# Kernel optimization log

Hardware: AMD Instinct MI355X
Metric: run time of the kernel (lower is better)

The kernel has to match this reference:

```python
import jax, jax.numpy as jnp
import numpy as np

BETA_MIN = 0.1
BETA_MAX = 20.0


def _Beta(t):
    # integral of linear beta schedule
    return BETA_MIN * t + 0.5 * (BETA_MAX - BETA_MIN) * t ** 2


def setup_inputs() -> dict:
    key = jax.random.key(0)
    k1, k2, k3, k4, k5 = jax.random.split(key, 5)
    B, K, D = 4096, 128, 256
    x = jax.random.normal(k1, (B, D), dtype=jnp.float32)
    t = jax.random.uniform(k2, (B,), dtype=jnp.float32)
    centers = jax.random.normal(k3, (K, D), dtype=jnp.float32)
    # keep stds positive and well-conditioned
    stds = 0.5 + 0.5 * jax.random.uniform(k4, (K, D), dtype=jnp.float32)
    # positive mixture weights (original only requires positivity, takes log)
    weights = 0.1 + jax.random.uniform(k5, (K,), dtype=jnp.float32)
    return {"x": x, "t": t, "centers": centers, "stds": stds, "weights": weights}


def reference(x, t, centers, stds, weights):
    ndim = centers.shape[1]

    def log_prob(xx):
        Bt = _Beta(t)[:, None, None]                 # [B,1,1]
        a = jnp.exp(-Bt / 2)
        centers_t = a * centers[None]                # [B,K,D]
        var_t = jnp.exp(-Bt) * stds[None] ** 2 + 1.0 - jnp.exp(-Bt)  # [B,K,D]
        diff = xx[:, None, :] - centers_t            # [B,K,D]
        # NOTE: faithful to source, which uses ndim/2 * sum(log(2*pi*var)) (not 1/2)
        lp = (-(diff ** 2) / (2.0 * var_t)).sum(-1) \
             - (ndim / 2) * jnp.log(2.0 * jnp.pi * var_t).sum(-1)    # [B,K]
        lp = lp + jnp.log(weights)[None, :]
        return jax.scipy.special.logsumexp(lp, axis=1)               # [B]

    grad_log_prob = jax.grad(lambda xx: log_prob(xx).sum())(x)       # [B,D]
    Bt = _Beta(t)[:, None]                                           # [B,1]
    return -jnp.sqrt(1.0 - jnp.exp(-Bt)) * grad_log_prob
```

## Files before the change

kernel.cpp:

```cpp
#include <hip/hip_runtime.h>
#include <math.h>


constexpr int Kc = 128;
constexpr int Dc = 256;
constexpr int G  = 2;

__global__ void prep_kernel(const float* __restrict__ centers,
                            const float* __restrict__ stds,
                            float* __restrict__ CT, float* __restrict__ AT) {
    int idx = blockIdx.x * blockDim.x + threadIdx.x;
    if (idx >= Kc * Dc) return;
    int d = idx >> 7;
    int k = idx & (Kc - 1);
    float c = centers[k * Dc + d];
    float s = stds[k * Dc + d];
    CT[idx] = c;
    AT[idx] = s * s - 1.0f;
}

__global__ __launch_bounds__(256) void score_kernel(
    const float* __restrict__ x, const float* __restrict__ t,
    const float* __restrict__ centers, const float* __restrict__ stds,
    const float* __restrict__ weights,
    const float* __restrict__ CT, const float* __restrict__ AT,
    float* __restrict__ out)
{
    const int b0  = blockIdx.x * G;
    const int tid = threadIdx.x;

    __shared__ float x_lds[G][Dc];
    __shared__ float part1[G][2][Kc];
    __shared__ float partL[G][2][Kc];
    __shared__ float pn[G][Kc];
    __shared__ float wmax[G][2];
    __shared__ float wsum[G][2];

    float e[G], na[G], onee[G], sg[G];
    #pragma unroll
    for (int g = 0; g < G; ++g) {
        float tt = t[b0 + g];
        float Bt = 0.1f * tt + 9.95f * tt * tt;
        float ee = expf(-Bt);
        e[g]    = ee;
        na[g]   = -sqrtf(ee);
        onee[g] = 1.0f - ee;
        sg[g]   = sqrtf(1.0f - ee);
    }

    #pragma unroll
    for (int g = 0; g < G; ++g)
        x_lds[g][tid] = x[(b0 + g) * Dc + tid];
    __syncthreads();

    const int kk    = tid & (Kc - 1);
    const int half  = tid >> 7;
    const int dbase = half * (Dc / 2);

    float acc1[G] = {0.0f, 0.0f};
    float accL[G] = {0.0f, 0.0f};
    for (int dd = 0; dd < Dc / 2; dd += 8) {
        float prod[G] = {1.0f, 1.0f};
        #pragma unroll
        for (int j = 0; j < 8; ++j) {
            int d   = dbase + dd + j;
            float c = CT[d * Kc + kk];
            float A = AT[d * Kc + kk];
            #pragma unroll
            for (int g = 0; g < G; ++g) {
                float var  = fmaf(e[g], A, 1.0f);
                float rv   = __builtin_amdgcn_rcpf(var);
                float diff = fmaf(na[g], c, x_lds[g][d]);
                acc1[g] = fmaf(diff * diff, rv, acc1[g]);
                prod[g] *= var;
            }
        }
        #pragma unroll
        for (int g = 0; g < G; ++g)
            accL[g] += __log2f(prod[g]);
    }
    #pragma unroll
    for (int g = 0; g < G; ++g) {
        part1[g][half][kk] = acc1[g];
        partL[g][half][kk] = accL[g];
    }
    __syncthreads();

    float lp[G], pe[G];
    if (tid < Kc) {
        float lw = __logf(weights[tid]);
        #pragma unroll
        for (int g = 0; g < G; ++g) {
            float S1 = part1[g][0][tid] + part1[g][1][tid];
            float S2 = partL[g][0][tid] + partL[g][1][tid];
            lp[g] = fmaf(-0.5f, S1, fmaf(-88.72283911167299f, S2, lw));
            float m = lp[g];
            #pragma unroll
            for (int off = 32; off > 0; off >>= 1)
                m = fmaxf(m, __shfl_xor(m, off, 64));
            if ((tid & 63) == 0) wmax[g][tid >> 6] = m;
        }
    }
    __syncthreads();
    if (tid < Kc) {
        #pragma unroll
        for (int g = 0; g < G; ++g) {
            float m = fmaxf(wmax[g][0], wmax[g][1]);
            pe[g] = exp2f((lp[g] - m) * 1.4426950408889634f);
            float s = pe[g];
            #pragma unroll
            for (int off = 32; off > 0; off >>= 1)
                s += __shfl_xor(s, off, 64);
            if ((tid & 63) == 0) wsum[g][tid >> 6] = s;
        }
    }
    __syncthreads();
    if (tid < Kc) {
        #pragma unroll
        for (int g = 0; g < G; ++g) {
            float Z = wsum[g][0] + wsum[g][1];
            pn[g][tid] = pe[g] * __builtin_amdgcn_rcpf(Z);
        }
    }
    __syncthreads();

    float xg[G], O[G] = {0.0f, 0.0f};
    #pragma unroll
    for (int g = 0; g < G; ++g) xg[g] = x_lds[g][tid];

    #pragma unroll 4
    for (int k = 0; k < Kc; ++k) {
        float c  = centers[k * Dc + tid];
        float sd = stds[k * Dc + tid];
        float s2 = sd * sd;
        #pragma unroll
        for (int g = 0; g < G; ++g) {
            float var  = fmaf(e[g], s2, onee[g]);
            float rv   = __builtin_amdgcn_rcpf(var);
            float diff = fmaf(na[g], c, xg[g]);
            O[g] = fmaf(pn[g][k], diff * rv, O[g]);
        }
    }
    #pragma unroll
    for (int g = 0; g < G; ++g)
        out[(b0 + g) * Dc + tid] = sg[g] * O[g];
}

extern "C" void kernel_launch(void* const* d_in, const int* in_sizes, int n_in,
                              void* d_out, int out_size, void* d_ws, size_t ws_size,
                              hipStream_t stream) {
    const float* x       = (const float*)d_in[0];
    const float* t       = (const float*)d_in[1];
    const float* centers = (const float*)d_in[2];
    const float* stds    = (const float*)d_in[3];
    const float* weights = (const float*)d_in[4];
    float* outp = (float*)d_out;

    float* CT = (float*)d_ws;
    float* AT = CT + Kc * Dc;

    const int B = in_sizes[1];

    prep_kernel<<<(Kc * Dc + 255) / 256, 256, 0, stream>>>(centers, stds, CT, AT);
    score_kernel<<<B / G, 256, 0, stream>>>(x, t, centers, stds, weights, CT, AT, outp);
}
```

Before: 123.2 us.

## Process four batch rows per block with vectorized loads and shared reciprocals

Raises rows per block from 2 to 4 so each load of centers and stds is reused across more batch rows. The prep kernel now writes float4-interleaved layouts so the first pass loads four d values per vector load, and x and the softmax weights are stored transposed in LDS for vector reads. Four reciprocals are merged into one by combining fractions over a common denominator, which cuts rcp instructions but risks overflow or precision loss in the product of denominators. Normalization by Z moves to the end, which drops a sync and the pn pass.

```diff
diff --git a/kernel.cpp b/kernel.cpp
--- a/kernel.cpp
+++ b/kernel.cpp
@@ -4,35 +4,38 @@
 
 constexpr int Kc = 128;
 constexpr int Dc = 256;
-constexpr int G  = 2;
+constexpr int G  = 4;
+
+typedef float f4 __attribute__((ext_vector_type(4)));
 
 __global__ void prep_kernel(const float* __restrict__ centers,
                             const float* __restrict__ stds,
-                            float* __restrict__ CT, float* __restrict__ AT) {
+                            float* __restrict__ CT4, float* __restrict__ AT4) {
     int idx = blockIdx.x * blockDim.x + threadIdx.x;
     if (idx >= Kc * Dc) return;
-    int d = idx >> 7;
-    int k = idx & (Kc - 1);
-    float c = centers[k * Dc + d];
-    float s = stds[k * Dc + d];
-    CT[idx] = c;
-    AT[idx] = s * s - 1.0f;
+    int k = idx >> 8;
+    int d = idx & (Dc - 1);
+    int o = (d >> 2) * (Kc * 4) + k * 4 + (d & 3);
+    float c = centers[idx];
+    float s = stds[idx];
+    CT4[o] = c;
+    AT4[o] = s * s - 1.0f;
 }
 
 __global__ __launch_bounds__(256) void score_kernel(
     const float* __restrict__ x, const float* __restrict__ t,
     const float* __restrict__ centers, const float* __restrict__ stds,
     const float* __restrict__ weights,
-    const float* __restrict__ CT, const float* __restrict__ AT,
+    const float* __restrict__ CT4, const float* __restrict__ AT4,
     float* __restrict__ out)
 {
     const int b0  = blockIdx.x * G;
     const int tid = threadIdx.x;
 
-    __shared__ float x_lds[G][Dc];
+    __shared__ __align__(16) float xT[Dc][G];
     __shared__ float part1[G][2][Kc];
     __shared__ float partL[G][2][Kc];
-    __shared__ float pn[G][Kc];
+    __shared__ __align__(16) float peT[Kc][G];
     __shared__ float wmax[G][2];
     __shared__ float wsum[G][2];
 
@@ -40,8 +43,8 @@
     #pragma unroll
     for (int g = 0; g < G; ++g) {
         float tt = t[b0 + g];
-        float Bt = 0.1f * tt + 9.95f * tt * tt;
-        float ee = expf(-Bt);
+        float Bt = fmaf(9.95f * tt, tt, 0.1f * tt);
+        float ee = __expf(-Bt);
         e[g]    = ee;
         na[g]   = -sqrtf(ee);
         onee[g] = 1.0f - ee;
@@ -50,29 +53,50 @@
 
     #pragma unroll
     for (int g = 0; g < G; ++g)
-        x_lds[g][tid] = x[(b0 + g) * Dc + tid];
+        xT[tid][g] = x[(b0 + g) * Dc + tid];
     __syncthreads();
 
     const int kk    = tid & (Kc - 1);
     const int half  = tid >> 7;
     const int dbase = half * (Dc / 2);
 
-    float acc1[G] = {0.0f, 0.0f};
-    float accL[G] = {0.0f, 0.0f};
-    for (int dd = 0; dd < Dc / 2; dd += 8) {
-        float prod[G] = {1.0f, 1.0f};
-        #pragma unroll
-        for (int j = 0; j < 8; ++j) {
-            int d   = dbase + dd + j;
-            float c = CT[d * Kc + kk];
-            float A = AT[d * Kc + kk];
+    const f4* CT4v = (const f4*)CT4;
+    const f4* AT4v = (const f4*)AT4;
+    const f4* xTv  = (const f4*)(&xT[0][0]);
+
+    float acc1[G] = {0.f, 0.f, 0.f, 0.f};
+    float accL[G] = {0.f, 0.f, 0.f, 0.f};
+
+    for (int grp = 0; grp < 8; ++grp) {
+        float prod[G] = {1.f, 1.f, 1.f, 1.f};
+        #pragma unroll
+        for (int q = 0; q < 4; ++q) {
+            const int d0 = dbase + (grp * 4 + q) * 4;
+            const int qi = (d0 >> 2) * Kc + kk;
+            f4 c4  = CT4v[qi];
+            f4 A4  = AT4v[qi];
+            f4 xv0 = xTv[d0 + 0];
+            f4 xv1 = xTv[d0 + 1];
+            f4 xv2 = xTv[d0 + 2];
+            f4 xv3 = xTv[d0 + 3];
             #pragma unroll
             for (int g = 0; g < G; ++g) {
-                float var  = fmaf(e[g], A, 1.0f);
-                float rv   = __builtin_amdgcn_rcpf(var);
-                float diff = fmaf(na[g], c, x_lds[g][d]);
-                acc1[g] = fmaf(diff * diff, rv, acc1[g]);
-                prod[g] *= var;
+                float v0 = fmaf(e[g], A4[0], 1.0f);
+                float v1 = fmaf(e[g], A4[1], 1.0f);
+                float v2 = fmaf(e[g], A4[2], 1.0f);
+                float v3 = fmaf(e[g], A4[3], 1.0f);
+                float f0 = fmaf(na[g], c4[0], xv0[g]);
+                float f1 = fmaf(na[g], c4[1], xv1[g]);
+                float f2 = fmaf(na[g], c4[2], xv2[g]);
+                float f3 = fmaf(na[g], c4[3], xv3[g]);
+                float s0 = f0 * f0, s1 = f1 * f1, s2 = f2 * f2, s3 = f3 * f3;
+                float d01 = v0 * v1, d23 = v2 * v3;
+                float n01 = s0 * v1; n01 = fmaf(s1, v0, n01);
+                float n23 = s2 * v3; n23 = fmaf(s3, v2, n23);
+                float den = d01 * d23;
+                float num = n01 * d23; num = fmaf(n23, d01, num);
+                acc1[g] = fmaf(num, __builtin_amdgcn_rcpf(den), acc1[g]);
+                prod[g] *= den;
             }
         }
         #pragma unroll
@@ -86,15 +110,15 @@
     }
     __syncthreads();
 
-    float lp[G], pe[G];
+    float lpv[G];
     if (tid < Kc) {
         float lw = __logf(weights[tid]);
         #pragma unroll
         for (int g = 0; g < G; ++g) {
             float S1 = part1[g][0][tid] + part1[g][1][tid];
             float S2 = partL[g][0][tid] + partL[g][1][tid];
-            lp[g] = fmaf(-0.5f, S1, fmaf(-88.72283911167299f, S2, lw));
-            float m = lp[g];
+            lpv[g] = fmaf(-0.5f, S1, fmaf(-88.72283911167299f, S2, lw));
+            float m = lpv[g];
             #pragma unroll
             for (int off = 32; off > 0; off >>= 1)
                 m = fmaxf(m, __shfl_xor(m, off, 64));
@@ -105,9 +129,10 @@
     if (tid < Kc) {
         #pragma unroll
         for (int g = 0; g < G; ++g) {
-            float m = fmaxf(wmax[g][0], wmax[g][1]);
-            pe[g] = exp2f((lp[g] - m) * 1.4426950408889634f);
-            float s = pe[g];
+            float m  = fmaxf(wmax[g][0], wmax[g][1]);
+            float pe = __expf(lpv[g] - m);
+            peT[tid][g] = pe;
+            float s = pe;
             #pragma unroll
             for (int off = 32; off > 0; off >>= 1)
                 s += __shfl_xor(s, off, 64);
@@ -115,35 +140,56 @@
         }
     }
     __syncthreads();
-    if (tid < Kc) {
+
+    f4 xvv = xTv[tid];
+    float O[G] = {0.f, 0.f, 0.f, 0.f};
+    const f4* peTv = (const f4*)(&peT[0][0]);
+    const float* cp = centers + tid;
+    const float* sp = stds + tid;
+
+    for (int kq = 0; kq < 32; ++kq) {
+        const int k0 = kq * 4;
+        float c0 = cp[(k0 + 0) * Dc];
+        float c1 = cp[(k0 + 1) * Dc];
+        float c2 = cp[(k0 + 2) * Dc];
+        float c3 = cp[(k0 + 3) * Dc];
+        float t0 = sp[(k0 + 0) * Dc];
+        float t1 = sp[(k0 + 1) * Dc];
+        float t2 = sp[(k0 + 2) * Dc];
+        float t3 = sp[(k0 + 3) * Dc];
+        f4 p0 = peTv[k0 + 0];
+        f4 p1 = peTv[k0 + 1];
+        f4 p2 = peTv[k0 + 2];
+        f4 p3 = peTv[k0 + 3];
+        float s20 = t0 * t0, s21 = t1 * t1, s22 = t2 * t2, s23 = t3 * t3;
         #pragma unroll
         for (int g = 0; g < G; ++g) {
-            float Z = wsum[g][0] + wsum[g][1];
-            pn[g][tid] = pe[g] * __builtin_amdgcn_rcpf(Z);
-        }
-    }
-    __syncthreads();
-
-    float xg[G], O[G] = {0.0f, 0.0f};
-    #pragma unroll
-    for (int g = 0; g < G; ++g) xg[g] = x_lds[g][tid];
-
-    #pragma unroll 4
-    for (int k = 0; k < Kc; ++k) {
-        float c  = centers[k * Dc + tid];
-        float sd = stds[k * Dc + tid];
-        float s2 = sd * sd;
-        #pragma unroll
-        for (int g = 0; g < G; ++g) {
-            float var  = fmaf(e[g], s2, onee[g]);
-            float rv   = __builtin_amdgcn_rcpf(var);
-            float diff = fmaf(na[g], c, xg[g]);
-            O[g] = fmaf(pn[g][k], diff * rv, O[g]);
-        }
-    }
-    #pragma unroll
-    for (int g = 0; g < G; ++g)
-        out[(b0 + g) * Dc + tid] = sg[g] * O[g];
+            float v0 = fmaf(e[g], s20, onee[g]);
+            float v1 = fmaf(e[g], s21, onee[g]);
+            float v2 = fmaf(e[g], s22, onee[g]);
+            float v3 = fmaf(e[g], s23, onee[g]);
+            float f0 = fmaf(na[g], c0, xvv[g]);
+            float f1 = fmaf(na[g], c1, xvv[g]);
+            float f2 = fmaf(na[g], c2, xvv[g]);
+            float f3 = fmaf(na[g], c3, xvv[g]);
+            float u0 = p0[g] * f0;
+            float u1 = p1[g] * f1;
+            float u2 = p2[g] * f2;
+            float u3 = p3[g] * f3;
+            float d01 = v0 * v1, d23 = v2 * v3;
+            float n01 = u0 * v1; n01 = fmaf(u1, v0, n01);
+            float n23 = u2 * v3; n23 = fmaf(u3, v2, n23);
+            float den = d01 * d23;
+            float num = n01 * d23; num = fmaf(n23, d01, num);
+            O[g] = fmaf(num, __builtin_amdgcn_rcpf(den), O[g]);
+        }
+    }
+
+    #pragma unroll
+    for (int g = 0; g < G; ++g) {
+        float Z = wsum[g][0] + wsum[g][1];
+        out[(b0 + g) * Dc + tid] = sg[g] * __builtin_amdgcn_rcpf(Z) * O[g];
+    }
 }
 
 extern "C" void kernel_launch(void* const* d_in, const int* in_sizes, int n_in,
@@ -156,11 +202,11 @@
     const float* weights = (const float*)d_in[4];
     float* outp = (float*)d_out;
 
-    float* CT = (float*)d_ws;
-    float* AT = CT + Kc * Dc;
+    float* CT4 = (float*)d_ws;
+    float* AT4 = CT4 + Kc * Dc;
 
     const int B = in_sizes[1];
 
-    prep_kernel<<<(Kc * Dc + 255) / 256, 256, 0, stream>>>(centers, stds, CT, AT);
-    score_kernel<<<B / G, 256, 0, stream>>>(x, t, centers, stds, weights, CT, AT, outp);
+    prep_kernel<<<(Kc * Dc + 255) / 256, 256, 0, stream>>>(centers, stds, CT4, AT4);
+    score_kernel<<<B / G, 256, 0, stream>>>(x, t, centers, stds, weights, CT4, AT4, outp);
 }
```

Measured after the change: 114.9 us. -6.7%, faster.
